# Optimization experiments

Measured on AMD Instinct MI355X. Metric: run time of the kernel, lower is better.

The kernel has to match this reference:

```python
import jax, jax.numpy as jnp
import numpy as np
import math

MAX_ATOMS = 50
B = 2048
D = 512            # node_hidden_dim
MA = 512           # mol_a_repr_dim
ATT = 128          # attention dim
HID = 256          # mlp hidden width


def _counts():
    return (np.arange(B) % MAX_ATOMS) + 1  # deterministic ragged counts, sum = 52176


def _lin_params(key, din, dout):
    k1, k2 = jax.random.split(key)
    lim = 1.0 / math.sqrt(din)
    w = jax.random.uniform(k1, (din, dout), jnp.float32, -lim, lim)
    b = jax.random.uniform(k2, (dout,), jnp.float32, -lim, lim)
    return w, b


def mlp2(x, w1, b1, w2, b2):
    # create_mlp(in, out, [hidden]) => Linear -> ReLU -> Linear
    return jax.nn.relu(x @ w1 + b1) @ w2 + b2


def setup_inputs() -> dict:
    key = jax.random.key(0)
    ks = jax.random.split(key, 16)
    counts = _counts()
    N = int(counts.sum())  # 52176
    inp = {
        'mol_a_reprs': jax.random.normal(ks[0], (B, MA), jnp.float32),
        'node_hiddens': jax.random.normal(ks[1], (N, D), jnp.float32),
        'batch_counts': jnp.asarray(counts, jnp.int32),
    }
    wq1, bq1 = _lin_params(ks[2], D, HID); wq2, bq2 = _lin_params(ks[3], HID, ATT)
    wk1, bk1 = _lin_params(ks[4], D, HID); wk2, bk2 = _lin_params(ks[5], HID, ATT)
    wv1, bv1 = _lin_params(ks[6], D, HID); wv2, bv2 = _lin_params(ks[7], HID, ATT)
    uk1, ubk1 = _lin_params(ks[8], ATT, HID); uk2, ubk2 = _lin_params(ks[9], HID, ATT)
    uq1, ubq1 = _lin_params(ks[10], MA, HID); uq2, ubq2 = _lin_params(ks[11], HID, ATT)
    cs1, bcs1 = _lin_params(ks[12], MAX_ATOMS, 128); cs2, bcs2 = _lin_params(ks[13], 128, MAX_ATOMS)
    inp.update(dict(wq1=wq1, bq1=bq1, wq2=wq2, bq2=bq2,
                    wk1=wk1, bk1=bk1, wk2=wk2, bk2=bk2,
                    wv1=wv1, bv1=bv1, wv2=wv2, bv2=bv2,
                    uk1=uk1, ubk1=ubk1, uk2=uk2, ubk2=ubk2,
                    uq1=uq1, ubq1=ubq1, uq2=uq2, ubq2=ubq2,
                    cs1=cs1, bcs1=bcs1, cs2=cs2, bcs2=bcs2))
    return inp


def reference(mol_a_reprs, node_hiddens, batch_counts,
              wq1, bq1, wq2, bq2, wk1, bk1, wk2, bk2, wv1, bv1, wv2, bv2,
              uk1, ubk1, uk2, ubk2, uq1, ubq1, uq2, ubq2,
              cs1, bcs1, cs2, bcs2):
    N = node_hiddens.shape[0]
    offsets = jnp.concatenate([jnp.zeros((1,), jnp.int32),
                               jnp.cumsum(batch_counts)[:-1].astype(jnp.int32)])
    pos = jnp.arange(MAX_ATOMS, dtype=jnp.int32)                     # (M,)
    valid = pos[None, :] < batch_counts[:, None]                      # (B, M)
    gidx = jnp.clip(offsets[:, None] + pos[None, :], 0, N - 1)        # (B, M)
    # ragged gather -> padded (B, M, D), zeros at pad slots
    inp = jnp.where(valid[:, :, None], node_hiddens[gidx], 0.0)
    mask = ~valid                                                     # True where padded

    K = mlp2(inp, wk1, bk1, wk2, bk2)                                 # (B, M, 128)
    Q = mlp2(inp, wq1, bq1, wq2, bq2)
    V = mlp2(inp, wv1, bv1, wv2, bv2)
    KQT = jnp.einsum('bmd,bnd->bmn', K, Q)                            # (B, M, M)
    KQT = jnp.where(mask[:, :, None] | mask[:, None, :], -1e9, KQT)
    attn = jax.nn.softmax(KQT / math.sqrt(ATT), axis=-1)
    corr = jnp.einsum('bmn,bnd->bmd', attn, V)                        # (B, M, 128)

    K2 = mlp2(corr, uk1, ubk1, uk2, ubk2)                             # (B, M, 128)
    Q2 = mlp2(mol_a_reprs, uq1, ubq1, uq2, ubq2)                      # (B, 128)
    logits = jnp.einsum('bmd,bd->bm', K2, Q2) / math.sqrt(ATT)        # (B, M)
    sel = jax.nn.sigmoid(mlp2(logits, cs1, bcs1, cs2, bcs2))          # (B, M)

    # ragged scatter back to (N,); pad slots routed to dummy slot N
    sidx = jnp.where(valid, offsets[:, None] + pos[None, :], N)
    out = jnp.zeros((N + 1,), sel.dtype).at[sidx.reshape(-1)].set(sel.reshape(-1))
    return out[:N]
```

## Files before the change

### kernel.cpp

```cpp
#include <hip/hip_runtime.h>
#include <hip/hip_bf16.h>
#include <math.h>

#define DIM   512
#define HIDW  256
#define ATTW  128
#define MAXC  50
#define BLK   256
#define PBLK  512
#define KW    128
#define HLW   128
#define HL2   264
#define BUFW  136
#define SB_W  52
#define CH    10
#define PXR   32
#define SCL   0.08838834764831845f

#define SWZ(row, e) ((e) ^ (((row) & 7) << 3))

#define AT_PA 12800
#define AT_KB 19200
#define AT_SM 32000

typedef float f32x4 __attribute__((ext_vector_type(4)));
typedef short s16x8 __attribute__((ext_vector_type(8)));

__device__ __forceinline__ float bf2f(ushort u){ union{unsigned i;float f;}v; v.i=((unsigned)u)<<16; return v.f; }
__device__ __forceinline__ ushort f2bf(float f){
  union{float f;unsigned i;}v; v.f=f;
  unsigned r = v.i + 0x7fffu + ((v.i>>16)&1u);
  return (ushort)(r>>16);
}
__device__ __forceinline__ s16x8 ldfrag(const ushort* p){ s16x8 v; __builtin_memcpy(&v, p, 16); return v; }
__device__ __forceinline__ f32x4 mfma16(s16x8 a, s16x8 b, f32x4 c){
  return __builtin_amdgcn_mfma_f32_16x16x32_bf16(a, b, c, 0, 0, 0);
}
__device__ __forceinline__ const ushort* fragp(const ushort* Wf, int ntile, int ktile, int KT, int L){
  return Wf + (((size_t)ntile*KT + ktile)*64 + L)*8;
}

template<bool F32>
__device__ __forceinline__ float ld(const void* p, int i){
  if (F32) return ((const float*)p)[i];
  return bf2f(((const ushort*)p)[i]);
}

struct P27 {
  const void *molA, *nodeH; const int* counts;
  const void *wq1,*bq1,*wq2,*bq2, *wk1,*bk1,*wk2,*bk2, *wv1,*bv1,*wv2,*bv2;
  const void *uk1,*ubk1,*uk2,*ubk2, *uq1,*ubq1,*uq2,*ubq2;
  const void *cs1,*bcs1,*cs2,*bcs2;
  void* out;
};

#define O_WK1T 0
#define O_WQ1T 131072
#define O_WV1T 262144
#define O_WK2T 393216
#define O_WQ2T 425984
#define O_WV2T 458752
#define O_UK1T 491520
#define O_UK2T 524288
#define WT_ELEMS   557056
#define O_UQ1TT 557056
#define O_UQ2TT 688128
#define WT2_ELEMS  720896
#define WT_T2ELEMS 393216
#define WT_BYTE_OFF 8704
#define Q2_BYTE_OFF (WT_BYTE_OFF + WT2_ELEMS*2)

__global__ void prep_kernel(const ushort* __restrict__ molAu,
                            const int* __restrict__ counts, int nb,
                            int* __restrict__ wsInt)
{
  __shared__ int part[BLK];
  __shared__ int cnt;
  const int t = threadIdx.x;
  if (t == 0) cnt = 0;
  __syncthreads();
  int e = (molAu[t] >> 7) & 0xFF;
  if (e >= 100 && e <= 140) atomicAdd(&cnt, 1);
  const int per = (nb + BLK - 1) / BLK;
  int s = 0;
  for (int i = 0; i < per; i++) { int idx = t*per + i; if (idx < nb) s += counts[idx]; }
  part[t] = s;
  __syncthreads();
  if (t == 0) {
    int run = 0;
    for (int i = 0; i < BLK; i++) { int v = part[i]; part[i] = run; run += v; }
    wsInt[0] = (cnt >= 220) ? 0 : 1;
  }
  __syncthreads();
  int run = part[t];
  for (int i = 0; i < per; i++) {
    int idx = t*per + i;
    if (idx < nb) { wsInt[4 + idx] = run; run += counts[idx]; }
  }
}

__global__ void transpose_wt(P27 P, const int* __restrict__ wsInt,
                             ushort* __restrict__ wt, unsigned long long cap_elems)
{
  unsigned i = blockIdx.x*BLK + threadIdx.x;
  if (i >= WT2_ELEMS) return;
  if ((unsigned long long)i >= cap_elems) return;
  const int f32m = wsInt[0];
  const void* src; unsigned j; int K, ldw;
  if (i < O_WK2T) {
    int m = i / 131072; j = i - m*131072;
    src = (m==0) ? P.wk1 : ((m==1) ? P.wq1 : P.wv1);
    K = 512; ldw = HIDW;
  } else if (i < O_UK1T) {
    int m = (i - O_WK2T) / 32768; j = (i - O_WK2T) - m*32768;
    src = (m==0) ? P.wk2 : ((m==1) ? P.wq2 : P.wv2);
    K = 256; ldw = ATTW;
  } else if (i < O_UK2T) {
    j = i - O_UK1T; src = P.uk1;  K = 128; ldw = HIDW;
  } else if (i < O_UQ1TT) {
    j = i - O_UK2T; src = P.uk2;  K = 256; ldw = ATTW;
  } else if (i < O_UQ2TT) {
    j = i - O_UQ1TT; src = P.uq1; K = 512; ldw = HIDW;
  } else {
    j = i - O_UQ2TT; src = P.uq2; K = 256; ldw = ATTW;
  }
  int tile = j >> 9, within = j & 511;
  int Lp = within >> 3, jj = within & 7;
  int l16 = Lp & 15, quad = Lp >> 4;
  int KT = K >> 5;
  int ntile = tile / KT, ktile = tile - ntile*KT;
  int n = ntile*16 + l16;
  int k = ktile*32 + quad*8 + jj;
  int idx = k*ldw + n;
  float v = f32m ? ((const float*)src)[idx] : bf2f(((const ushort*)src)[idx]);
  wt[i] = f2bf(v);
}

__global__ void __launch_bounds__(PBLK, 6)
proj_kernel(P27 P, const int* __restrict__ wsInt, const ushort* __restrict__ wt,
            ushort* __restrict__ kqv, float* __restrict__ q2ws,
            long Nrows, int nb, int ntX)
{
  __shared__ __align__(16) ushort xs [PXR*DIM];
  __shared__ __align__(16) ushort hid[PXR*HIDW];
  const int t = threadIdx.x, bid = blockIdx.x;
  const int f32m = wsInt[0];
  const long NP = Nrows * ATTW;
  const bool isml = (bid >= ntX);
  const long r0 = isml ? (long)(bid - ntX)*PXR : (long)bid*PXR;
  int rows;
  const void* X;
  if (isml) { int rem = nb - (int)r0;        rows = (rem < PXR) ? rem : PXR; X = P.molA; }
  else      { long rem = Nrows - r0;         rows = (rem < PXR) ? (int)rem : PXR; X = P.nodeH; }
  if (rows <= 0) return;

  for (int i = t*8; i < PXR*DIM; i += PBLK*8) {
    int row = i >> 9;
    int e   = i & (DIM-1);
    s16x8 o = {};
    if (row < rows) {
      if (f32m) {
        const float* xp = (const float*)X + (r0 + row)*DIM + e;
        f32x4 v0, v1; __builtin_memcpy(&v0, xp, 16); __builtin_memcpy(&v1, xp+4, 16);
#pragma unroll
        for (int q = 0; q < 4; q++) { o[q] = (short)f2bf(v0[q]); o[4+q] = (short)f2bf(v1[q]); }
      } else {
        o = ldfrag((const ushort*)X + (r0 + row)*DIM + e);
      }
    }
    __builtin_memcpy(&xs[row*DIM + SWZ(row, e)], &o, 16);
  }
  __syncthreads();

  const int w = t >> 6, L = t & 63, quad = L >> 4, l16 = L & 15;
  const int nsets = isml ? 1 : 3;
  for (int si = 0; si < nsets; si++) {
    const ushort *W1t, *W2t; const void *b1, *b2;
    if (isml)        { W1t = wt+O_UQ1TT; b1 = P.ubq1; W2t = wt+O_UQ2TT; b2 = P.ubq2; }
    else if (si==0)  { W1t = wt+O_WK1T;  b1 = P.bk1;  W2t = wt+O_WK2T;  b2 = P.bk2;  }
    else if (si==1)  { W1t = wt+O_WQ1T;  b1 = P.bq1;  W2t = wt+O_WQ2T;  b2 = P.bq2;  }
    else             { W1t = wt+O_WV1T;  b1 = P.bv1;  W2t = wt+O_WV2T;  b2 = P.bv2;  }

    f32x4 acc[2][2];
#pragma unroll
    for (int i = 0; i < 2; i++) { acc[i][0] = (f32x4){0.f,0.f,0.f,0.f}; acc[i][1] = (f32x4){0.f,0.f,0.f,0.f}; }
#pragma unroll 2
    for (int k0 = 0; k0 < DIM; k0 += 32) {
      const int kt = k0 >> 5;
      const int eo = SWZ(l16, k0 + quad*8);
      s16x8 a0 = ldfrag(xs + l16*DIM + eo);
      s16x8 a1 = ldfrag(xs + (16 + l16)*DIM + eo);
      s16x8 b0 = ldfrag(fragp(W1t, w*2,     kt, 16, L));
      s16x8 b1v= ldfrag(fragp(W1t, w*2 + 1, kt, 16, L));
      acc[0][0] = mfma16(a0, b0,  acc[0][0]);
      acc[0][1] = mfma16(a0, b1v, acc[0][1]);
      acc[1][0] = mfma16(a1, b0,  acc[1][0]);
      acc[1][1] = mfma16(a1, b1v, acc[1][1]);
    }
    __syncthreads();
#pragma unroll
    for (int nt = 0; nt < 2; nt++) {
      int col = w*32 + nt*16 + l16;
      float bb = f32m ? ((const float*)b1)[col] : bf2f(((const ushort*)b1)[col]);
#pragma unroll
      for (int mt = 0; mt < 2; mt++)
#pragma unroll
        for (int r = 0; r < 4; r++) {
          int row = mt*16 + quad*4 + r;
          hid[row*HIDW + SWZ(row, col)] = f2bf(fmaxf(acc[mt][nt][r] + bb, 0.f));
        }
    }
    __syncthreads();

    f32x4 acc2[2];
    acc2[0] = (f32x4){0.f,0.f,0.f,0.f}; acc2[1] = (f32x4){0.f,0.f,0.f,0.f};
#pragma unroll 2
    for (int k0 = 0; k0 < HIDW; k0 += 32) {
      const int kt = k0 >> 5;
      const int eo = SWZ(l16, k0 + quad*8);
      s16x8 a0 = ldfrag(hid + l16*HIDW + eo);
      s16x8 a1 = ldfrag(hid + (16 + l16)*HIDW + eo);
      s16x8 b0 = ldfrag(fragp(W2t, w, kt, 8, L));
      acc2[0] = mfma16(a0, b0, acc2[0]);
      acc2[1] = mfma16(a1, b0, acc2[1]);
    }
    {
      int col = w*16 + l16;
      float bb = f32m ? ((const float*)b2)[col] : bf2f(((const ushort*)b2)[col]);
#pragma unroll
      for (int mt = 0; mt < 2; mt++)
#pragma unroll
        for (int r = 0; r < 4; r++) {
          int row = mt*16 + quad*4 + r;
          if (row < rows) {
            float v = acc2[mt][r] + bb;
            if (isml) q2ws[(r0 + row)*ATTW + col] = v;
            else      kqv[(size_t)si*NP + (r0 + row)*ATTW + col] = f2bf(v);
          }
        }
    }
  }
}


__device__ __forceinline__ void scores_g(const ushort* __restrict__ Kp,
                                         const ushort* __restrict__ Qp,
                                         long offset, int c,
                                         float* __restrict__ sb, int t)
{
  const int w = t >> 6, L = t & 63, quad = L >> 4, l16 = L & 15;
  f32x4 acc[4];
#pragma unroll
  for (int i = 0; i < 4; i++) acc[i] = (f32x4){0.f,0.f,0.f,0.f};
  const int col = w*16 + l16;
  const long gq = offset + ((col < c) ? col : 0);
  long ga[4];
#pragma unroll
  for (int mt = 0; mt < 4; mt++) {
    int row = mt*16 + l16;
    ga[mt] = offset + ((row < c) ? row : 0);
  }
#pragma unroll
  for (int k0 = 0; k0 < ATTW; k0 += 32) {
    s16x8 b = ldfrag(Qp + (size_t)gq*ATTW + k0 + quad*8);
#pragma unroll
    for (int mt = 0; mt < 4; mt++) {
      s16x8 a = ldfrag(Kp + (size_t)ga[mt]*ATTW + k0 + quad*8);
      acc[mt] = mfma16(a, b, acc[mt]);
    }
  }
#pragma unroll
  for (int mt = 0; mt < 4; mt++)
#pragma unroll
    for (int r = 0; r < 4; r++) {
      int row = mt*16 + quad*4 + r;
      if (row < MAXC && col < MAXC)
        sb[row*SB_W + col] = (row < c && col < c) ? acc[mt][r]*SCL : -1e9f*SCL;
    }
}

__device__ __forceinline__ void softmax_pa(float* __restrict__ sb,
                                           ushort* __restrict__ pa, int c, int t)
{
  const int m = t >> 2, j = t & 3;
  if (m < MAXC) {
    float* row = sb + m*SB_W;
    float mx = -3.4e38f;
    for (int n = j; n < MAXC; n += 4) mx = fmaxf(mx, row[n]);
    mx = fmaxf(mx, __shfl_xor(mx, 1));
    mx = fmaxf(mx, __shfl_xor(mx, 2));
    float sum = 0.f;
    for (int n = j; n < MAXC; n += 4) { float e = expf(row[n] - mx); row[n] = e; sum += e; }
    sum += __shfl_xor(sum, 1);
    sum += __shfl_xor(sum, 2);
    float inv = 1.f / sum;
    for (int n = j; n < 64; n += 4)
      pa[m*64 + SWZ(m, n)] = (n < MAXC) ? f2bf(row[n] * inv) : (ushort)0;
  }
}

__device__ __forceinline__ void corr_half(const ushort* __restrict__ pa,
                                          const ushort* __restrict__ vt,
                                          ushort* __restrict__ dst, int colbase, int t)
{
  const int w = t >> 6, L = t & 63, quad = L >> 4, l16 = L & 15;
  f32x4 acc[4];
#pragma unroll
  for (int i = 0; i < 4; i++) acc[i] = (f32x4){0.f,0.f,0.f,0.f};
  const int dr = w*16 + l16;
#pragma unroll
  for (int k0 = 0; k0 < 64; k0 += 32) {
    s16x8 b = ldfrag(vt + dr*64 + SWZ(dr, k0 + quad*8));
#pragma unroll
    for (int mt = 0; mt < 4; mt++) {
      int row = mt*16 + l16;
      int ar = (row < MAXC) ? row : 0;
      s16x8 a = ldfrag(pa + ar*64 + SWZ(ar, k0 + quad*8));
      acc[mt] = mfma16(a, b, acc[mt]);
    }
  }
  const int col = colbase + w*16 + l16;
#pragma unroll
  for (int mt = 0; mt < 4; mt++)
#pragma unroll
    for (int r = 0; r < 4; r++) {
      int row = mt*16 + quad*4 + r;
      if (row < MAXC)
        dst[row*KW + SWZ(row, col)] = f2bf(acc[mt][r]);
    }
}

template<bool F32>
__device__ __forceinline__ void s1l_half(const ushort* __restrict__ src,
                                         const ushort* __restrict__ W1t,
                                         const void* __restrict__ Bv,
                                         ushort* __restrict__ hl, int t, int h)
{
  const int w = t >> 6, L = t & 63, quad = L >> 4, l16 = L & 15;
  f32x4 acc[4][2];
#pragma unroll
  for (int i = 0; i < 4; i++) { acc[i][0] = (f32x4){0.f,0.f,0.f,0.f}; acc[i][1] = (f32x4){0.f,0.f,0.f,0.f}; }
#pragma unroll
  for (int k0 = 0; k0 < ATTW; k0 += 32) {
    const int kt = k0 >> 5;
    s16x8 b0 = ldfrag(fragp(W1t, h*8 + w*2,     kt, 4, L));
    s16x8 b1 = ldfrag(fragp(W1t, h*8 + w*2 + 1, kt, 4, L));
#pragma unroll
    for (int mt = 0; mt < 4; mt++) {
      int row = mt*16 + l16;
      int ar = (row < MAXC) ? row : 0;
      s16x8 a = ldfrag(src + ar*KW + SWZ(ar, k0 + quad*8));
      acc[mt][0] = mfma16(a, b0, acc[mt][0]);
      acc[mt][1] = mfma16(a, b1, acc[mt][1]);
    }
  }
#pragma unroll
  for (int nt = 0; nt < 2; nt++) {
    int lcol = w*32 + nt*16 + l16;
    float bb = ld<F32>(Bv, h*128 + lcol);
#pragma unroll
    for (int mt = 0; mt < 4; mt++)
#pragma unroll
      for (int r = 0; r < 4; r++) {
        int row = mt*16 + quad*4 + r;
        if (row < MAXC)
          hl[row*HLW + SWZ(row, lcol)] = f2bf(fmaxf(acc[mt][nt][r] + bb, 0.f));
      }
  }
}

template<bool F32>
__device__ __forceinline__ void s2_partial(const ushort* __restrict__ hl,
                                           const ushort* __restrict__ W2t,
                                           int h, f32x4 (&acc)[4][2], int t)
{
  const int w = t >> 6, L = t & 63, quad = L >> 4, l16 = L & 15;
#pragma unroll
  for (int k0 = 0; k0 < 128; k0 += 32) {
    const int kt = h*4 + (k0 >> 5);
    s16x8 b0 = ldfrag(fragp(W2t, w*2,     kt, 8, L));
    s16x8 b1 = ldfrag(fragp(W2t, w*2 + 1, kt, 8, L));
#pragma unroll
    for (int mt = 0; mt < 4; mt++) {
      int row = mt*16 + l16;
      int ar = (row < MAXC) ? row : 0;
      s16x8 a = ldfrag(hl + ar*HLW + SWZ(ar, k0 + quad*8));
      acc[mt][0] = mfma16(a, b0, acc[mt][0]);
      acc[mt][1] = mfma16(a, b1, acc[mt][1]);
    }
  }
}

template<bool F32>
__device__ __forceinline__ void s2_store(f32x4 (&acc)[4][2], const void* __restrict__ Bv,
                                         ushort* __restrict__ dst, int t)
{
  const int w = t >> 6, L = t & 63, quad = L >> 4, l16 = L & 15;
#pragma unroll
  for (int nt = 0; nt < 2; nt++) {
    int col = w*32 + nt*16 + l16;
    float bb = ld<F32>(Bv, col);
#pragma unroll
    for (int mt = 0; mt < 4; mt++)
#pragma unroll
      for (int r = 0; r < 4; r++) {
        int row = mt*16 + quad*4 + r;
        if (row < MAXC)
          dst[row*KW + SWZ(row, col)] = f2bf(acc[mt][nt][r] + bb);
      }
  }
}

template<bool F32>
__device__ void attn_body(const P27& P, int b, int t, char* smem,
                          long offset, int c,
                          const ushort* __restrict__ wt,
                          const ushort* __restrict__ Kp, const ushort* __restrict__ Qp,
                          const ushort* __restrict__ Vp, const float* __restrict__ q2ws)
{
  float*  sb = (float*)smem;
  ushort* vt = (ushort*)smem;
  ushort* hl = (ushort*)smem;
  ushort* pa = (ushort*)(smem + AT_PA);
  ushort* kb = (ushort*)(smem + AT_KB);
  float* q2   = (float*)smem;
  float* lgt  = (float*)(smem + 512);
  float* selh = (float*)(smem + 768);

  scores_g(Kp, Qp, offset, c, sb, t);
  __syncthreads();
  softmax_pa(sb, pa, c, t);
  __syncthreads();

#pragma unroll
  for (int half = 0; half < 2; half++) {
    for (int i = t; i < 512; i += BLK) {
      int atom = i & 63, chunk = i >> 6;
      s16x8 f = {};
      if (atom < c) f = ldfrag(Vp + (size_t)(offset + atom)*ATTW + half*64 + chunk*8);
#pragma unroll
      for (int j = 0; j < 8; j++) {
        int d = chunk*8 + j;
        vt[d*64 + SWZ(d, atom)] = (ushort)f[j];
      }
    }
    __syncthreads();
    corr_half(pa, vt, kb, half*64, t);
    __syncthreads();
  }

  {
    f32x4 acc[4][2];
#pragma unroll
    for (int i = 0; i < 4; i++) { acc[i][0] = (f32x4){0.f,0.f,0.f,0.f}; acc[i][1] = (f32x4){0.f,0.f,0.f,0.f}; }
    s1l_half<F32>(kb, wt + O_UK1T, P.ubk1, hl, t, 0); __syncthreads();
    s2_partial<F32>(hl, wt + O_UK2T, 0, acc, t);      __syncthreads();
    s1l_half<F32>(kb, wt + O_UK1T, P.ubk1, hl, t, 1); __syncthreads();
    s2_partial<F32>(hl, wt + O_UK2T, 1, acc, t);
    s2_store<F32>(acc, P.ubk2, kb, t);
    __syncthreads();
  }

  if (t < ATTW) q2[t] = q2ws[(size_t)b*ATTW + t];
  __syncthreads();
  if (t < MAXC) {
    float s = 0.f;
    for (int k = 0; k < ATTW; k++)
      s += bf2f(kb[t*KW + SWZ(t, k)]) * q2[k];
    lgt[t] = s * SCL;
  }
  __syncthreads();
  if (t < ATTW) {
    float a = 0.f;
    for (int k = 0; k < MAXC; k++)
      a += lgt[k] * ld<F32>(P.cs1, k*ATTW + t);
    selh[t] = fmaxf(a + ld<F32>(P.bcs1, t), 0.f);
  }
  __syncthreads();
  if (t < c) {
    float a = 0.f;
    for (int k = 0; k < ATTW; k++)
      a += selh[k] * ld<F32>(P.cs2, k*MAXC + t);
    a += ld<F32>(P.bcs2, t);
    float v = 1.f / (1.f + expf(-a));
    if (F32) ((float*)P.out)[offset + t] = v;
    else     ((ushort*)P.out)[offset + t] = f2bf(v);
  }
}

__global__ void __launch_bounds__(BLK, 5)
attn_kernel(P27 P, const int* __restrict__ wsInt, const ushort* __restrict__ wt,
            const ushort* __restrict__ kqv, const float* __restrict__ q2ws, long Nrows)
{
  __shared__ __align__(16) char smem[AT_SM];
  const int t = threadIdx.x, b = blockIdx.x;
  const int f32m = wsInt[0];
  const long offset = wsInt[4 + b];
  const int c = P.counts[b];
  const long NP = Nrows * ATTW;
  const ushort* Kp = kqv;
  const ushort* Qp = kqv + NP;
  const ushort* Vp = kqv + 2*NP;
  if (f32m) attn_body<true >(P, b, t, smem, offset, c, wt, Kp, Qp, Vp, q2ws);
  else      attn_body<false>(P, b, t, smem, offset, c, wt, Kp, Qp, Vp, q2ws);
}

template<bool F32, bool XB>
__device__ __forceinline__ void stage1_mfma(const void* __restrict__ X, int xb, int c,
                                            const ushort* __restrict__ Wt,
                                            const void* __restrict__ Bv,
                                            ushort* __restrict__ hl, int hls, int t,
                                            int wlim)
{
  const int w = t >> 6, L = t & 63, quad = L >> 4, l16 = L & 15;
  f32x4 acc[4][4];
#pragma unroll
  for (int i = 0; i < 4; i++)
#pragma unroll
    for (int j = 0; j < 4; j++) acc[i][j] = (f32x4){0.f,0.f,0.f,0.f};

  bool va[4]; int rr[4];
#pragma unroll
  for (int mt = 0; mt < 4; mt++) {
    int row = mt*16 + l16;
    va[mt] = (row < c);
    rr[mt] = va[mt] ? row : 0;
  }

#pragma unroll 2
  for (int k0 = 0; k0 < DIM; k0 += 32) {
    const int kt = k0 >> 5;
    s16x8 a[4];
#pragma unroll
    for (int mt = 0; mt < 4; mt++) {
      s16x8 z = {};
      if (va[mt]) {
        if (XB || !F32) {
          a[mt] = ldfrag((const ushort*)X + xb + rr[mt]*DIM + k0 + quad*8);
        } else {
          const float* xp = (const float*)X + xb + rr[mt]*DIM + k0 + quad*8;
          f32x4 v0, v1;
          __builtin_memcpy(&v0, xp, 16);
          __builtin_memcpy(&v1, xp+4, 16);
          s16x8 v;
#pragma unroll
          for (int j = 0; j < 4; j++) { v[j] = (short)f2bf(v0[j]); v[4+j] = (short)f2bf(v1[j]); }
          a[mt] = v;
        }
      } else a[mt] = z;
    }
#pragma unroll
    for (int nt = 0; nt < 4; nt++) {
      s16x8 b = ldfrag(fragp(Wt, w*4 + nt, kt, 16, L));
#pragma unroll
      for (int mt = 0; mt < 4; mt++)
        acc[mt][nt] = mfma16(a[mt], b, acc[mt][nt]);
    }
  }
#pragma unroll
  for (int nt = 0; nt < 4; nt++) {
    int col = w*64 + nt*16 + l16;
    float bb = ld<F32>(Bv, col);
#pragma unroll
    for (int mt = 0; mt < 4; mt++)
#pragma unroll
      for (int r = 0; r < 4; r++) {
        int row = mt*16 + quad*4 + r;
        if (row < wlim)
          hl[row*hls + col] = f2bf(fmaxf(acc[mt][nt][r] + bb, 0.f));
      }
  }
}

template<bool F32>
__device__ void stage1_g(const void* X, int xb, int c,
                         const void* W, const void* Bv, ushort* hl, int t)
{
  for (int r0 = 0; r0 < MAXC; r0 += CH) {
    float acc[CH];
#pragma unroll
    for (int i = 0; i < CH; i++) acc[i] = 0.f;
    for (int k = 0; k < DIM; k++) {
      float wv = ld<F32>(W, k*HIDW + t);
#pragma unroll
      for (int i = 0; i < CH; i++) {
        int m = r0 + i;
        int mc = (m < c) ? m : 0;
        float xv = ld<F32>(X, xb + mc*DIM + k);
        acc[i] += ((m < c) ? xv : 0.f) * wv;
      }
    }
    float bb = ld<F32>(Bv, t);
#pragma unroll
    for (int i = 0; i < CH; i++)
      hl[(r0+i)*HIDW + t] = f2bf(fmaxf(acc[i] + bb, 0.f));
  }
}

template<bool F32>
__device__ void stage1_l(const ushort* S, const void* W, const void* Bv,
                         ushort* hl, int t)
{
  for (int r0 = 0; r0 < MAXC; r0 += CH) {
    float acc[CH];
#pragma unroll
    for (int i = 0; i < CH; i++) acc[i] = 0.f;
    for (int k = 0; k < ATTW; k++) {
      float wv = ld<F32>(W, k*HIDW + t);
#pragma unroll
      for (int i = 0; i < CH; i++)
        acc[i] += bf2f(S[(r0+i)*BUFW + k]) * wv;
    }
    float bb = ld<F32>(Bv, t);
#pragma unroll
    for (int i = 0; i < CH; i++)
      hl[(r0+i)*HIDW + t] = f2bf(fmaxf(acc[i] + bb, 0.f));
  }
}

template<bool F32>
__device__ void stage2(const void* W, const void* Bv, const ushort* hlp,
                       ushort* dst, int t)
{
  const int col = t & (ATTW-1);
  const int h = t >> 7;
  float bb = ld<F32>(Bv, col);
  for (int m = h; m < MAXC; m += 2) {
    float a = 0.f;
    for (int k = 0; k < HIDW; k++)
      a += bf2f(hlp[m*HIDW + k]) * ld<F32>(W, k*ATTW + col);
    dst[m*BUFW + col] = f2bf(a + bb);
  }
}

template<bool F32, bool MF>
__device__ void body(const P27& P, int b, int t,
                     ushort* hl, ushort* buf0, ushort* buf1, float* sb,
                     float* q2h, float* q2, float* logit, float* selh,
                     int offset, int c, const ushort* wt)
{
  const int xb = offset * DIM;

  if (MF) stage1_mfma<F32,false>(P.nodeH, xb, c, wt + O_WK1T, P.bk1, hl, HIDW, t, MAXC);
  else    stage1_g<F32>(P.nodeH, xb, c, P.wk1, P.bk1, hl, t);
  __syncthreads();
  stage2<F32>(P.wk2, P.bk2, hl, buf0, t);
  __syncthreads();
  if (MF) stage1_mfma<F32,false>(P.nodeH, xb, c, wt + O_WQ1T, P.bq1, hl, HIDW, t, MAXC);
  else    stage1_g<F32>(P.nodeH, xb, c, P.wq1, P.bq1, hl, t);
  __syncthreads();
  stage2<F32>(P.wq2, P.bq2, hl, buf1, t);
  __syncthreads();

  for (int idx = t; idx < MAXC*MAXC; idx += BLK) {
    int m = idx / MAXC, n = idx - m*MAXC;
    float s;
    if (m < c && n < c) {
      s = 0.f;
      for (int k = 0; k < ATTW; k++)
        s += bf2f(buf0[m*BUFW + k]) * bf2f(buf1[n*BUFW + k]);
    } else s = -1e9f;
    sb[m*SB_W + n] = s * SCL;
  }
  __syncthreads();
  if (t < MAXC) {
    float* row = sb + t*SB_W;
    float mx = row[0];
    for (int n = 1; n < MAXC; n++) mx = fmaxf(mx, row[n]);
    float sum = 0.f;
    for (int n = 0; n < MAXC; n++) { float e = expf(row[n] - mx); row[n] = e; sum += e; }
    float inv = 1.f / sum;
    for (int n = 0; n < MAXC; n++) row[n] *= inv;
  }
  __syncthreads();

  if (MF) stage1_mfma<F32,false>(P.nodeH, xb, c, wt + O_WV1T, P.bv1, hl, HIDW, t, MAXC);
  else    stage1_g<F32>(P.nodeH, xb, c, P.wv1, P.bv1, hl, t);
  __syncthreads();
  stage2<F32>(P.wv2, P.bv2, hl, buf0, t);
  __syncthreads();

  {
    const int col = t & (ATTW-1);
    const int h = t >> 7;
    for (int m = h; m < MAXC; m += 2) {
      float a = 0.f;
      for (int n = 0; n < MAXC; n++)
        a += sb[m*SB_W + n] * bf2f(buf0[n*BUFW + col]);
      buf1[m*BUFW + col] = f2bf(a);
    }
  }
  __syncthreads();

  stage1_l<F32>(buf1, P.uk1, P.ubk1, hl, t);
  __syncthreads();
  stage2<F32>(P.uk2, P.ubk2, hl, buf0, t);
  __syncthreads();

  {
    float a = 0.f;
    for (int k = 0; k < DIM; k++)
      a += ld<F32>(P.molA, b*DIM + k) * ld<F32>(P.uq1, k*HIDW + t);
    q2h[t] = fmaxf(a + ld<F32>(P.ubq1, t), 0.f);
  }
  __syncthreads();
  if (t < ATTW) {
    float a = 0.f;
    for (int k = 0; k < HIDW; k++)
      a += q2h[k] * ld<F32>(P.uq2, k*ATTW + t);
    q2[t] = a + ld<F32>(P.ubq2, t);
  }
  __syncthreads();
  if (t < MAXC) {
    float s = 0.f;
    for (int k = 0; k < ATTW; k++)
      s += bf2f(buf0[t*BUFW + k]) * q2[k];
    logit[t] = s * SCL;
  }
  __syncthreads();
  if (t < ATTW) {
    float a = 0.f;
    for (int k = 0; k < MAXC; k++)
      a += logit[k] * ld<F32>(P.cs1, k*ATTW + t);
    selh[t] = fmaxf(a + ld<F32>(P.bcs1, t), 0.f);
  }
  __syncthreads();
  if (t < c) {
    float a = 0.f;
    for (int k = 0; k < ATTW; k++)
      a += selh[k] * ld<F32>(P.cs2, k*MAXC + t);
    a += ld<F32>(P.bcs2, t);
    float v = 1.f / (1.f + expf(-a));
    if (F32) ((float*)P.out)[offset + t] = v;
    else     ((ushort*)P.out)[offset + t] = f2bf(v);
  }
}

__global__ void fused_mfma(P27 P, const int* __restrict__ wsInt, const ushort* __restrict__ wt)
{
  __shared__ __align__(16) ushort hl  [MAXC*HIDW];
  __shared__ __align__(16) ushort buf0[MAXC*BUFW];
  __shared__ __align__(16) ushort buf1[MAXC*BUFW];
  __shared__ __align__(16) float  sb  [MAXC*SB_W];
  __shared__ __align__(16) float  q2h [HIDW];
  __shared__ __align__(16) float  q2  [ATTW];
  __shared__ __align__(16) float  logit[64];
  __shared__ __align__(16) float  selh[ATTW];
  const int t = threadIdx.x, b = blockIdx.x;
  const int f32m = wsInt[0];
  const int offset = wsInt[4 + b];
  const int c = P.counts[b];
  if (f32m) body<true , true>(P, b, t, hl, buf0, buf1, sb, q2h, q2, logit, selh, offset, c, wt);
  else      body<false, true>(P, b, t, hl, buf0, buf1, sb, q2h, q2, logit, selh, offset, c, wt);
}

__global__ void fused_scalar(P27 P, const int* __restrict__ wsInt)
{
  __shared__ __align__(16) ushort hl  [MAXC*HIDW];
  __shared__ __align__(16) ushort buf0[MAXC*BUFW];
  __shared__ __align__(16) ushort buf1[MAXC*BUFW];
  __shared__ __align__(16) float  sb  [MAXC*SB_W];
  __shared__ __align__(16) float  q2h [HIDW];
  __shared__ __align__(16) float  q2  [ATTW];
  __shared__ __align__(16) float  logit[64];
  __shared__ __align__(16) float  selh[ATTW];
  const int t = threadIdx.x, b = blockIdx.x;
  const int f32m = wsInt[0];
  const int offset = wsInt[4 + b];
  const int c = P.counts[b];
  if (f32m) body<true , false>(P, b, t, hl, buf0, buf1, sb, q2h, q2, logit, selh, offset, c, nullptr);
  else      body<false, false>(P, b, t, hl, buf0, buf1, sb, q2h, q2, logit, selh, offset, c, nullptr);
}

extern "C" void kernel_launch(void* const* d_in, const int* in_sizes, int n_in,
                              void* d_out, int out_size, void* d_ws, size_t ws_size,
                              hipStream_t stream) {
  P27 P;
  P.molA  = d_in[0];
  P.nodeH = d_in[1];
  P.counts= (const int*)d_in[2];
  P.wq1 = d_in[3];  P.bq1 = d_in[4];  P.wq2 = d_in[5];  P.bq2 = d_in[6];
  P.wk1 = d_in[7];  P.bk1 = d_in[8];  P.wk2 = d_in[9];  P.bk2 = d_in[10];
  P.wv1 = d_in[11]; P.bv1 = d_in[12]; P.wv2 = d_in[13]; P.bv2 = d_in[14];
  P.uk1 = d_in[15]; P.ubk1= d_in[16]; P.uk2 = d_in[17]; P.ubk2= d_in[18];
  P.uq1 = d_in[19]; P.ubq1= d_in[20]; P.uq2 = d_in[21]; P.ubq2= d_in[22];
  P.cs1 = d_in[23]; P.bcs1= d_in[24]; P.cs2 = d_in[25]; P.bcs2= d_in[26];
  P.out = d_out;
  const int nb = in_sizes[2];
  int* wsInt = (int*)d_ws;

  prep_kernel<<<dim3(1), dim3(BLK), 0, stream>>>((const ushort*)d_in[0],
                                                 (const int*)d_in[2], nb, wsInt);

  const long xelems = (long)in_sizes[1];
  const long Nrows  = xelems / DIM;
  const int  ntX = (int)((Nrows + PXR - 1) / PXR);
  const int  ntA = (nb + PXR - 1) / PXR;

  size_t q2_off  = (size_t)Q2_BYTE_OFF;
  size_t kqv_off = (q2_off + (size_t)nb * ATTW * 4 + 255) & ~(size_t)255;
  const size_t need_new = kqv_off + (size_t)3 * Nrows * ATTW * 2;
  const size_t need2    = (size_t)WT_BYTE_OFF + (size_t)WT_T2ELEMS * 2;

  if (ws_size >= need_new) {
    ushort* wt   = (ushort*)((char*)d_ws + WT_BYTE_OFF);
    float*  q2ws = (float*)((char*)d_ws + q2_off);
    ushort* kqv  = (ushort*)((char*)d_ws + kqv_off);
    unsigned long long cap = (ws_size - WT_BYTE_OFF) / 2;
    transpose_wt<<<dim3((WT2_ELEMS + BLK - 1)/BLK), dim3(BLK), 0, stream>>>(P, wsInt, wt, cap);
    proj_kernel<<<dim3(ntX + ntA), dim3(PBLK), 0, stream>>>(P, wsInt, wt, kqv, q2ws,
                                                            Nrows, nb, ntX);
    attn_kernel<<<dim3(nb), dim3(BLK), 0, stream>>>(P, wsInt, wt, kqv, q2ws, Nrows);
  } else if (ws_size >= need2) {
    ushort* wt = (ushort*)((char*)d_ws + WT_BYTE_OFF);
    unsigned long long cap = (ws_size - WT_BYTE_OFF) / 2;
    transpose_wt<<<dim3((WT2_ELEMS + BLK - 1)/BLK), dim3(BLK), 0, stream>>>(P, wsInt, wt, cap);
    fused_mfma<<<dim3(nb), dim3(BLK), 0, stream>>>(P, wsInt, wt);
  } else {
    fused_scalar<<<dim3(nb), dim3(BLK), 0, stream>>>(P, wsInt);
  }
}
```

Before: 408.3 us.

## Double projection row tile and split hidden layer into two halves

```diff
diff --git a/kernel.cpp b/kernel.cpp
--- a/kernel.cpp
+++ b/kernel.cpp
@@ -14,7 +14,7 @@
 #define BUFW  136
 #define SB_W  52
 #define CH    10
-#define PXR   32
+#define PXR   64
 #define SCL   0.08838834764831845f
 
 #define SWZ(row, e) ((e) ^ (((row) & 7) << 3))
@@ -136,13 +136,13 @@
   wt[i] = f2bf(v);
 }
 
-__global__ void __launch_bounds__(PBLK, 6)
+__global__ void __launch_bounds__(PBLK, 4)
 proj_kernel(P27 P, const int* __restrict__ wsInt, const ushort* __restrict__ wt,
             ushort* __restrict__ kqv, float* __restrict__ q2ws,
             long Nrows, int nb, int ntX)
 {
   __shared__ __align__(16) ushort xs [PXR*DIM];
-  __shared__ __align__(16) ushort hid[PXR*HIDW];
+  __shared__ __align__(16) ushort hid[PXR*128];
   const int t = threadIdx.x, bid = blockIdx.x;
   const int f32m = wsInt[0];
   const long NP = Nrows * ATTW;
@@ -150,8 +150,8 @@
   const long r0 = isml ? (long)(bid - ntX)*PXR : (long)bid*PXR;
   int rows;
   const void* X;
-  if (isml) { int rem = nb - (int)r0;        rows = (rem < PXR) ? rem : PXR; X = P.molA; }
-  else      { long rem = Nrows - r0;         rows = (rem < PXR) ? (int)rem : PXR; X = P.nodeH; }
+  if (isml) { int rem = nb - (int)r0;  rows = (rem < PXR) ? rem : PXR;       X = P.molA; }
+  else      { long rem = Nrows - r0;   rows = (rem < PXR) ? (int)rem : PXR;  X = P.nodeH; }
   if (rows <= 0) return;
 
   for (int i = t*8; i < PXR*DIM; i += PBLK*8) {
@@ -181,54 +181,60 @@
     else if (si==1)  { W1t = wt+O_WQ1T;  b1 = P.bq1;  W2t = wt+O_WQ2T;  b2 = P.bq2;  }
     else             { W1t = wt+O_WV1T;  b1 = P.bv1;  W2t = wt+O_WV2T;  b2 = P.bv2;  }
 
-    f32x4 acc[2][2];
-#pragma unroll
-    for (int i = 0; i < 2; i++) { acc[i][0] = (f32x4){0.f,0.f,0.f,0.f}; acc[i][1] = (f32x4){0.f,0.f,0.f,0.f}; }
+    f32x4 acc2[4];
+#pragma unroll
+    for (int i = 0; i < 4; i++) acc2[i] = (f32x4){0.f,0.f,0.f,0.f};
+
+#pragma unroll
+    for (int h = 0; h < 2; h++) {
+      f32x4 acc[4];
+#pragma unroll
+      for (int i = 0; i < 4; i++) acc[i] = (f32x4){0.f,0.f,0.f,0.f};
 #pragma unroll 2
-    for (int k0 = 0; k0 < DIM; k0 += 32) {
-      const int kt = k0 >> 5;
-      const int eo = SWZ(l16, k0 + quad*8);
-      s16x8 a0 = ldfrag(xs + l16*DIM + eo);
-      s16x8 a1 = ldfrag(xs + (16 + l16)*DIM + eo);
-      s16x8 b0 = ldfrag(fragp(W1t, w*2,     kt, 16, L));
-      s16x8 b1v= ldfrag(fragp(W1t, w*2 + 1, kt, 16, L));
-      acc[0][0] = mfma16(a0, b0,  acc[0][0]);
-      acc[0][1] = mfma16(a0, b1v, acc[0][1]);
-      acc[1][0] = mfma16(a1, b0,  acc[1][0]);
-      acc[1][1] = mfma16(a1, b1v, acc[1][1]);
-    }
-    __syncthreads();
-#pragma unroll
-    for (int nt = 0; nt < 2; nt++) {
-      int col = w*32 + nt*16 + l16;
-      float bb = f32m ? ((const float*)b1)[col] : bf2f(((const ushort*)b1)[col]);
-#pragma unroll
-      for (int mt = 0; mt < 2; mt++)
-#pragma unroll
-        for (int r = 0; r < 4; r++) {
-          int row = mt*16 + quad*4 + r;
-          hid[row*HIDW + SWZ(row, col)] = f2bf(fmaxf(acc[mt][nt][r] + bb, 0.f));
+      for (int k0 = 0; k0 < DIM; k0 += 32) {
+        const int kt = k0 >> 5;
+        s16x8 b0 = ldfrag(fragp(W1t, h*8 + w, kt, 16, L));
+#pragma unroll
+        for (int mt = 0; mt < 4; mt++) {
+          int row = mt*16 + l16;
+          s16x8 a = ldfrag(xs + row*DIM + SWZ(row, k0 + quad*8));
+          acc[mt] = mfma16(a, b0, acc[mt]);
         }
-    }
-    __syncthreads();
-
-    f32x4 acc2[2];
-    acc2[0] = (f32x4){0.f,0.f,0.f,0.f}; acc2[1] = (f32x4){0.f,0.f,0.f,0.f};
-#pragma unroll 2
-    for (int k0 = 0; k0 < HIDW; k0 += 32) {
-      const int kt = k0 >> 5;
-      const int eo = SWZ(l16, k0 + quad*8);
-      s16x8 a0 = ldfrag(hid + l16*HIDW + eo);
-      s16x8 a1 = ldfrag(hid + (16 + l16)*HIDW + eo);
-      s16x8 b0 = ldfrag(fragp(W2t, w, kt, 8, L));
-      acc2[0] = mfma16(a0, b0, acc2[0]);
-      acc2[1] = mfma16(a1, b0, acc2[1]);
-    }
+      }
+      __syncthreads();
+      {
+        int lcol = w*16 + l16;
+        float bb = ld<true>(b1, 0) * 0.f;
+        bb = f32m ? ((const float*)b1)[h*128 + lcol] : bf2f(((const ushort*)b1)[h*128 + lcol]);
+#pragma unroll
+        for (int mt = 0; mt < 4; mt++)
+#pragma unroll
+          for (int r = 0; r < 4; r++) {
+            int row = mt*16 + quad*4 + r;
+            hid[row*128 + SWZ(row, lcol)] = f2bf(fmaxf(acc[mt][r] + bb, 0.f));
+          }
+      }
+      __syncthreads();
+
+#pragma unroll
+      for (int k0 = 0; k0 < 128; k0 += 32) {
+        const int kt = h*4 + (k0 >> 5);
+        s16x8 b0 = ldfrag(fragp(W2t, w, kt, 8, L));
+#pragma unroll
+        for (int mt = 0; mt < 4; mt++) {
+          int row = mt*16 + l16;
+          s16x8 a = ldfrag(hid + row*128 + SWZ(row, k0 + quad*8));
+          acc2[mt] = mfma16(a, b0, acc2[mt]);
+        }
+      }
+      if (h == 0) __syncthreads();
+    }
+
     {
       int col = w*16 + l16;
       float bb = f32m ? ((const float*)b2)[col] : bf2f(((const ushort*)b2)[col]);
 #pragma unroll
-      for (int mt = 0; mt < 2; mt++)
+      for (int mt = 0; mt < 4; mt++)
 #pragma unroll
         for (int r = 0; r < 4; r++) {
           int row = mt*16 + quad*4 + r;
@@ -239,6 +245,7 @@
           }
         }
     }
+    if (si + 1 < nsets) __syncthreads();
   }
 }
 
```

Result: slower. 424.0 us (+3.9%).
